# Kernel optimization log

Measured on AMD Instinct MI355X. Metric: run time of the kernel, lower is better.

Reference implementation:

```python
import jax, jax.numpy as jnp
import numpy as np

IN_F = 3072
OUT_F = 3072
SCALE = 1.0
KRON_SIZES = (16, 16, 12)  # q1*q2*q3 == IN_F


def setup_inputs() -> dict:
    key = jax.random.key(0)
    ks = jax.random.split(key, 8)
    x = jax.random.normal(ks[0], (4, 4096, IN_F), dtype=jnp.float32)
    # SVD factors of the frozen linear weight (k = min(out, in) = 3072)
    U = jax.random.normal(ks[1], (OUT_F, OUT_F), dtype=jnp.float32) * 0.02
    S = jax.random.uniform(ks[2], (OUT_F,), dtype=jnp.float32)  # nonnegative singular values
    V = jax.random.normal(ks[3], (OUT_F, IN_F), dtype=jnp.float32) * 0.02
    delta = jnp.full((OUT_F,), 0.001, dtype=jnp.float32)
    q1, q2, q3 = KRON_SIZES
    # initialized as identity in the module; add tiny noise so grads are nontrivial
    Q1 = jnp.eye(q1, dtype=jnp.float32) + 0.01 * jax.random.normal(ks[4], (q1, q1), dtype=jnp.float32)
    Q2 = jnp.eye(q2, dtype=jnp.float32) + 0.01 * jax.random.normal(ks[5], (q2, q2), dtype=jnp.float32)
    Q3 = jnp.eye(q3, dtype=jnp.float32) + 0.01 * jax.random.normal(ks[6], (q3, q3), dtype=jnp.float32)
    return {"x": x, "U": U, "S": S, "V": V, "delta": delta, "Q1": Q1, "Q2": Q2, "Q3": Q3}


def reference(x, U, S, V, delta, Q1, Q2, Q3):
    # S' = relu(S + delta); W = U @ diag(S') @ V  (diag fused as column scaling)
    Sp = jax.nn.relu(S + delta)
    W = (U * Sp[None, :]) @ V                      # [out, in]
    ortho = jnp.kron(jnp.kron(Q1, Q2), Q3)         # [in, in]
    W_t = ortho @ W.T                              # [in, out]
    # F.linear(input, W_t.t()) == input @ W_t ; dropout_p = 0 (inference)
    out = jnp.einsum('bsd,do->bso', x, W_t)
    return out * SCALE
```

## Files before the change

### kernel.cpp

```cpp
#include <hip/hip_runtime.h>

typedef unsigned short u16;
typedef unsigned int u32;
typedef __attribute__((ext_vector_type(8))) __bf16 bf16x8;
typedef __attribute__((ext_vector_type(4))) float f32x4;
typedef __attribute__((ext_vector_type(8))) u16 u16x8;


__device__ __forceinline__ u16 f2bf(float f) {
    union { float f; u32 u; } v; v.f = f;
    u32 r = v.u + 0x7FFFu + ((v.u >> 16) & 1u);
    return (u16)(r >> 16);
}

__device__ __forceinline__ void gload16(const void* g, void* l) {
    __builtin_amdgcn_global_load_lds(
        (const __attribute__((address_space(1))) u32*)g,
        (__attribute__((address_space(3))) u32*)l,
        16, 0, 0);
}

__global__ __launch_bounds__(256) void conv_bf16(
    const float* __restrict__ in, u16* __restrict__ out) {
    const size_t i = (size_t)blockIdx.x * 256 + threadIdx.x;
    const float4 a = ((const float4*)in)[i * 2];
    const float4 b = ((const float4*)in)[i * 2 + 1];
    u16x8 o;
    o[0] = f2bf(a.x); o[1] = f2bf(a.y); o[2] = f2bf(a.z); o[3] = f2bf(a.w);
    o[4] = f2bf(b.x); o[5] = f2bf(b.y); o[6] = f2bf(b.z); o[7] = f2bf(b.w);
    ((u16x8*)out)[i] = o;
}

__global__ __launch_bounds__(64) void conv_scale(
    const float* __restrict__ U, const float* __restrict__ S,
    const float* __restrict__ D, u16* __restrict__ out) {
    const int m = blockIdx.y;
    const int k = (blockIdx.x * 64 + threadIdx.x) * 8;
    const size_t base = (size_t)m * 3072 + k;
    const float4 a = *(const float4*)&U[base];
    const float4 b = *(const float4*)&U[base + 4];
    const float4 s1 = *(const float4*)&S[k], s2 = *(const float4*)&S[k + 4];
    const float4 d1 = *(const float4*)&D[k], d2 = *(const float4*)&D[k + 4];
    u16x8 o;
    o[0] = f2bf(a.x * fmaxf(s1.x + d1.x, 0.f));
    o[1] = f2bf(a.y * fmaxf(s1.y + d1.y, 0.f));
    o[2] = f2bf(a.z * fmaxf(s1.z + d1.z, 0.f));
    o[3] = f2bf(a.w * fmaxf(s1.w + d1.w, 0.f));
    o[4] = f2bf(b.x * fmaxf(s2.x + d2.x, 0.f));
    o[5] = f2bf(b.y * fmaxf(s2.y + d2.y, 0.f));
    o[6] = f2bf(b.z * fmaxf(s2.z + d2.z, 0.f));
    o[7] = f2bf(b.w * fmaxf(s2.w + d2.w, 0.f));
    *(u16x8*)&out[base] = o;
}

__global__ __launch_bounds__(256) void transpose_conv(
    const float* __restrict__ V, u16* __restrict__ Vt, int n) {
    __shared__ float tile[64][65];
    const int k0 = blockIdx.y * 64, j0 = blockIdx.x * 64;
    const int t = threadIdx.x;
    const int r = t >> 4, c4 = t & 15;
#pragma unroll
    for (int i = 0; i < 4; i++) {
        int row = i * 16 + r;
        const float4 v = *(const float4*)&V[(size_t)(k0 + row) * n + j0 + c4 * 4];
        tile[row][c4 * 4 + 0] = v.x;
        tile[row][c4 * 4 + 1] = v.y;
        tile[row][c4 * 4 + 2] = v.z;
        tile[row][c4 * 4 + 3] = v.w;
    }
    __syncthreads();
#pragma unroll
    for (int i = 0; i < 4; i++) {
        int row = i * 16 + r;
        ushort4 o;
        o.x = f2bf(tile[c4 * 4 + 0][row]);
        o.y = f2bf(tile[c4 * 4 + 1][row]);
        o.z = f2bf(tile[c4 * 4 + 2][row]);
        o.w = f2bf(tile[c4 * 4 + 3][row]);
        *(ushort4*)&Vt[(size_t)(j0 + row) * n + k0 + c4 * 4] = o;
    }
}

__global__ __launch_bounds__(512, 2) void gemm256(
    const u16* __restrict__ A, const u16* __restrict__ B,
    float* __restrict__ C, int M, int N, int K) {
    __shared__ u16 As[2][16384];
    __shared__ u16 Bs[2][16384];
    const int t = threadIdx.x;

    const int nbx = gridDim.x;
    const int bid = blockIdx.y * nbx + blockIdx.x;
    const int cpx = (nbx * gridDim.y) >> 3;
    const int sid = (bid & 7) * cpx + (bid >> 3);
    const int m0 = (sid / nbx) * 256, n0 = (sid % nbx) * 256;

    const int lane = t & 63, quad = lane >> 4, lrow = lane & 15;
    const int wave = t >> 6, wr = wave >> 2, wc = wave & 3;

    const int schunk = (t & 7) ^ ((t >> 3) & 7);
    const u16* Ag = A + (size_t)(m0 + (t >> 3)) * K + schunk * 8;
    const u16* Bg = B + (size_t)(n0 + (t >> 3)) * K + schunk * 8;

    const int sl = quad ^ (lrow & 7);
    const int aoff = (wr * 128 + lrow) * 64 + sl * 8;
    const int boff = (wc * 64 + lrow) * 64 + sl * 8;

    f32x4 acc[8][4] = {};

#define STGA(dst, q, kbe) gload16(Ag + (size_t)(q) * 64 * K + (kbe), (char*)(dst) + (q) * 8192 + t * 16)
#define STGB(dst, q, kbe) gload16(Bg + (size_t)(q) * 64 * K + (kbe), (char*)(dst) + (q) * 8192 + t * 16)

    const int NT = K >> 6;
    STGA(As[0], 0, 0); STGA(As[0], 1, 0); STGA(As[0], 2, 0); STGA(As[0], 3, 0);
    STGB(Bs[0], 0, 0); STGB(Bs[0], 1, 0); STGB(Bs[0], 2, 0); STGB(Bs[0], 3, 0);
    if (NT > 1) {
        STGA(As[1], 0, 64); STGA(As[1], 2, 64);
        STGB(Bs[1], 0, 64); STGB(Bs[1], 1, 64);
        asm volatile("s_waitcnt vmcnt(4)" ::: "memory");
    } else {
        asm volatile("s_waitcnt vmcnt(0)" ::: "memory");
    }
    __builtin_amdgcn_s_barrier();

    for (int tt = 0; tt < NT; ++tt) {
        const int b = tt & 1;
        const u16* Acur = As[b];
        const u16* Bcur = Bs[b];
        u16* Anxt = As[b ^ 1];
        u16* Bnxt = Bs[b ^ 1];
        bf16x8 bq[4], aq[4];

#define PHASE_TAIL(OFF)                                                       \
        __builtin_amdgcn_s_barrier();                                         \
        asm volatile("s_waitcnt lgkmcnt(0)" ::: "memory");                    \
        __builtin_amdgcn_sched_barrier(0);                                    \
        __builtin_amdgcn_s_setprio(1);                                        \
        _Pragma("unroll")                                                     \
        for (int mi = 0; mi < 4; mi++)                                        \
            _Pragma("unroll")                                                 \
            for (int ni = 0; ni < 4; ni++)                                    \
                acc[mi + OFF][ni] = __builtin_amdgcn_mfma_f32_16x16x32_bf16(  \
                    aq[mi], bq[ni], acc[mi + OFF][ni], 0, 0, 0);              \
        __builtin_amdgcn_s_setprio(0);

#pragma unroll
        for (int ni = 0; ni < 4; ni++) bq[ni] = *(const bf16x8*)&Bcur[boff + ni * 1024];
#pragma unroll
        for (int mi = 0; mi < 4; mi++) aq[mi] = *(const bf16x8*)&Acur[aoff + mi * 1024];
        if (tt + 1 < NT) { STGA(Anxt, 1, (tt + 1) * 64); STGA(Anxt, 3, (tt + 1) * 64); }
        PHASE_TAIL(0)
        __builtin_amdgcn_s_barrier();

#pragma unroll
        for (int mi = 0; mi < 4; mi++) aq[mi] = *(const bf16x8*)&Acur[aoff + (mi + 4) * 1024];
        if (tt + 1 < NT) { STGB(Bnxt, 2, (tt + 1) * 64); STGB(Bnxt, 3, (tt + 1) * 64); }
        PHASE_TAIL(4)
        __builtin_amdgcn_s_barrier();

#pragma unroll
        for (int ni = 0; ni < 4; ni++) bq[ni] = *(const bf16x8*)&Bcur[(boff + ni * 1024) ^ 32];
#pragma unroll
        for (int mi = 0; mi < 4; mi++) aq[mi] = *(const bf16x8*)&Acur[(aoff + mi * 1024) ^ 32];
        PHASE_TAIL(0)
        __builtin_amdgcn_s_barrier();

#pragma unroll
        for (int mi = 0; mi < 4; mi++) aq[mi] = *(const bf16x8*)&Acur[(aoff + (mi + 4) * 1024) ^ 32];
        if (tt + 2 < NT) {
            STGA((u16*)Acur, 0, (tt + 2) * 64); STGA((u16*)Acur, 2, (tt + 2) * 64);
            STGB((u16*)Bcur, 0, (tt + 2) * 64); STGB((u16*)Bcur, 1, (tt + 2) * 64);
        }
        PHASE_TAIL(4)
        if (tt + 2 < NT)
            asm volatile("s_waitcnt vmcnt(4)" ::: "memory");
        else
            asm volatile("s_waitcnt vmcnt(0)" ::: "memory");
        __builtin_amdgcn_s_barrier();
#undef PHASE_TAIL
    }
#undef STGA
#undef STGB

#pragma unroll
    for (int mi = 0; mi < 8; mi++) {
#pragma unroll
        for (int rr = 0; rr < 4; rr++) {
            const int row = m0 + wr * 128 + mi * 16 + quad * 4 + rr;
            float* cp = C + (size_t)row * N + n0 + wc * 64 + lrow;
#pragma unroll
            for (int ni = 0; ni < 4; ni++) cp[ni * 16] = acc[mi][ni][rr];
        }
    }
}

__global__ __launch_bounds__(256) void kron_apply(
    const float* __restrict__ W, const float* __restrict__ Q1,
    const float* __restrict__ Q2, const float* __restrict__ Q3,
    u16* __restrict__ WtT) {
    __shared__ float T0[3072], T1[3072];
    __shared__ float Q1s[256], Q2s[256], Q3s[144];
    const int o = blockIdx.x, t = threadIdx.x;
#pragma unroll
    for (int i = 0; i < 12; i++) T0[t + i * 256] = W[(size_t)o * 3072 + t + i * 256];
    Q1s[t] = Q1[t];
    Q2s[t] = Q2[t];
    if (t < 144) Q3s[t] = Q3[t];
    __syncthreads();
#pragma unroll
    for (int i = 0; i < 12; i++) {
        int e = t + i * 256;
        int d1 = e / 192, rem = e % 192;
        float s = 0.f;
#pragma unroll
        for (int j1 = 0; j1 < 16; j1++) s += Q1s[d1 * 16 + j1] * T0[j1 * 192 + rem];
        T1[e] = s;
    }
    __syncthreads();
#pragma unroll
    for (int i = 0; i < 12; i++) {
        int e = t + i * 256;
        int j3 = e % 12, d2 = (e / 12) & 15, d1 = e / 192;
        float s = 0.f;
#pragma unroll
        for (int j2 = 0; j2 < 16; j2++) s += Q2s[d2 * 16 + j2] * T1[d1 * 192 + j2 * 12 + j3];
        T0[e] = s;
    }
    __syncthreads();
#pragma unroll
    for (int i = 0; i < 12; i++) {
        int e = t + i * 256;
        int d3 = e % 12, b = e - d3;
        float s = 0.f;
#pragma unroll
        for (int j3 = 0; j3 < 12; j3++) s += Q3s[d3 * 12 + j3] * T0[b + j3];
        WtT[(size_t)o * 3072 + e] = f2bf(s);
    }
}

extern "C" void kernel_launch(void* const* d_in, const int* in_sizes, int n_in,
                              void* d_out, int out_size, void* d_ws, size_t ws_size,
                              hipStream_t stream) {
    const float* x   = (const float*)d_in[0];
    const float* U   = (const float*)d_in[1];
    const float* S   = (const float*)d_in[2];
    const float* V   = (const float*)d_in[3];
    const float* dl  = (const float*)d_in[4];
    const float* Q1  = (const float*)d_in[5];
    const float* Q2  = (const float*)d_in[6];
    const float* Q3  = (const float*)d_in[7];
    float* out = (float*)d_out;

    char* ws = (char*)d_ws;
    u16*   xb  = (u16*)ws;
    u16*   Ub  = (u16*)(ws + 100663296);
    u16*   Vt  = (u16*)(ws + 100663296 + 18874368);
    float* W   = (float*)(ws + 100663296 + 2 * 18874368);
    u16*   WtT = Ub;

    hipLaunchKernelGGL(conv_bf16, dim3(24576), dim3(256), 0, stream, x, xb);
    hipLaunchKernelGGL(conv_scale, dim3(6, 3072), dim3(64), 0, stream, U, S, dl, Ub);
    hipLaunchKernelGGL(transpose_conv, dim3(48, 48), dim3(256), 0, stream, V, Vt, 3072);
    hipLaunchKernelGGL(gemm256, dim3(12, 12), dim3(512), 0, stream,
                       Ub, Vt, W, 3072, 3072, 3072);
    hipLaunchKernelGGL(kron_apply, dim3(3072), dim3(256), 0, stream, W, Q1, Q2, Q3, WtT);
    hipLaunchKernelGGL(gemm256, dim3(12, 64), dim3(512), 0, stream,
                       xb, WtT, out, 16384, 3072, 3072);
}
```

Before: 850.1 us.

## Fuse fp32-to-bf16 conversion of x into main GEMM A-tile loads

Drops the separate conversion kernel that wrote a bf16 copy of x. The main GEMM now loads fp32 x tiles into registers, converts them, and writes them to LDS while the current tile's MFMAs run. B tiles keep the async global-to-LDS path. The weight-building GEMM is also moved to a simpler 128x128 single-buffered kernel with a larger grid. The fused path reads twice the bytes of A per tile and adds register pressure, VALU conversion work and explicit LDS writes inside the pipelined loop.

```diff
diff --git a/kernel.cpp b/kernel.cpp
--- a/kernel.cpp
+++ b/kernel.cpp
@@ -20,15 +20,11 @@
         16, 0, 0);
 }
 
-__global__ __launch_bounds__(256) void conv_bf16(
-    const float* __restrict__ in, u16* __restrict__ out) {
-    const size_t i = (size_t)blockIdx.x * 256 + threadIdx.x;
-    const float4 a = ((const float4*)in)[i * 2];
-    const float4 b = ((const float4*)in)[i * 2 + 1];
+__device__ __forceinline__ void cvt_wr(u16* dst, float4 a, float4 b) {
     u16x8 o;
     o[0] = f2bf(a.x); o[1] = f2bf(a.y); o[2] = f2bf(a.z); o[3] = f2bf(a.w);
     o[4] = f2bf(b.x); o[5] = f2bf(b.y); o[6] = f2bf(b.z); o[7] = f2bf(b.w);
-    ((u16x8*)out)[i] = o;
+    *(u16x8*)dst = o;
 }
 
 __global__ __launch_bounds__(64) void conv_scale(
@@ -81,8 +77,64 @@
     }
 }
 
-__global__ __launch_bounds__(512, 2) void gemm256(
+__global__ __launch_bounds__(256) void gemm_bt(
     const u16* __restrict__ A, const u16* __restrict__ B,
+    float* __restrict__ C, int M, int N, int K) {
+    __shared__ u16 As[128 * 64];
+    __shared__ u16 Bs[128 * 64];
+    const int t = threadIdx.x;
+    const int m0 = blockIdx.y * 128, n0 = blockIdx.x * 128;
+    const int wave = t >> 6, lane = t & 63;
+    const int quad = lane >> 4, lrow = lane & 15;
+    const int wm = (wave >> 1) * 64, wn = (wave & 1) * 64;
+    const int gr = t >> 3;
+    const int gc = (t & 7) ^ (gr & 7);
+    const int c0 = (quad ^ (lrow & 7)) * 8;
+    f32x4 acc[4][4] = {};
+
+    const u16* Ag = A + (size_t)(m0 + gr) * K + gc * 8;
+    const u16* Bg = B + (size_t)(n0 + gr) * K + gc * 8;
+
+    for (int kb = 0; kb < K; kb += 64) {
+#pragma unroll
+        for (int i = 0; i < 4; i++) {
+            gload16(Ag + (size_t)i * 32 * K + kb, (char*)As + i * 4096 + t * 16);
+            gload16(Bg + (size_t)i * 32 * K + kb, (char*)Bs + i * 4096 + t * 16);
+        }
+        __syncthreads();
+#pragma unroll
+        for (int kk = 0; kk < 2; kk++) {
+            const int co = c0 ^ (kk * 32);
+            bf16x8 af[4], bfr[4];
+#pragma unroll
+            for (int mi = 0; mi < 4; mi++)
+                af[mi] = *(const bf16x8*)&As[(wm + mi * 16 + lrow) * 64 + co];
+#pragma unroll
+            for (int ni = 0; ni < 4; ni++)
+                bfr[ni] = *(const bf16x8*)&Bs[(wn + ni * 16 + lrow) * 64 + co];
+#pragma unroll
+            for (int mi = 0; mi < 4; mi++)
+#pragma unroll
+                for (int ni = 0; ni < 4; ni++)
+                    acc[mi][ni] = __builtin_amdgcn_mfma_f32_16x16x32_bf16(
+                        af[mi], bfr[ni], acc[mi][ni], 0, 0, 0);
+        }
+        __syncthreads();
+    }
+#pragma unroll
+    for (int mi = 0; mi < 4; mi++) {
+#pragma unroll
+        for (int rr = 0; rr < 4; rr++) {
+            int row = m0 + wm + mi * 16 + quad * 4 + rr;
+            float* cp = C + (size_t)row * N + n0 + wn + lrow;
+#pragma unroll
+            for (int ni = 0; ni < 4; ni++) cp[ni * 16] = acc[mi][ni][rr];
+        }
+    }
+}
+
+__global__ __launch_bounds__(512, 2) void gemm256_xa(
+    const float* __restrict__ A, const u16* __restrict__ B,
     float* __restrict__ C, int M, int N, int K) {
     __shared__ u16 As[2][16384];
     __shared__ u16 Bs[2][16384];
@@ -98,8 +150,8 @@
     const int wave = t >> 6, wr = wave >> 2, wc = wave & 3;
 
     const int schunk = (t & 7) ^ ((t >> 3) & 7);
-    const u16* Ag = A + (size_t)(m0 + (t >> 3)) * K + schunk * 8;
-    const u16* Bg = B + (size_t)(n0 + (t >> 3)) * K + schunk * 8;
+    const float* Axf = A + (size_t)(m0 + (t >> 3)) * K + schunk * 8;
+    const u16*   Bg  = B + (size_t)(n0 + (t >> 3)) * K + schunk * 8;
 
     const int sl = quad ^ (lrow & 7);
     const int aoff = (wr * 128 + lrow) * 64 + sl * 8;
@@ -107,28 +159,32 @@
 
     f32x4 acc[8][4] = {};
 
-#define STGA(dst, q, kbe) gload16(Ag + (size_t)(q) * 64 * K + (kbe), (char*)(dst) + (q) * 8192 + t * 16)
 #define STGB(dst, q, kbe) gload16(Bg + (size_t)(q) * 64 * K + (kbe), (char*)(dst) + (q) * 8192 + t * 16)
 
     const int NT = K >> 6;
-    STGA(As[0], 0, 0); STGA(As[0], 1, 0); STGA(As[0], 2, 0); STGA(As[0], 3, 0);
     STGB(Bs[0], 0, 0); STGB(Bs[0], 1, 0); STGB(Bs[0], 2, 0); STGB(Bs[0], 3, 0);
-    if (NT > 1) {
-        STGA(As[1], 0, 64); STGA(As[1], 2, 64);
-        STGB(Bs[1], 0, 64); STGB(Bs[1], 1, 64);
-        asm volatile("s_waitcnt vmcnt(4)" ::: "memory");
-    } else {
-        asm volatile("s_waitcnt vmcnt(0)" ::: "memory");
-    }
+    if (NT > 1) { STGB(Bs[1], 0, 64); STGB(Bs[1], 1, 64); }
+#pragma unroll
+    for (int q = 0; q < 4; q++) {
+        const float* p = Axf + (size_t)q * 64 * K;
+        float4 x0 = *(const float4*)p;
+        float4 x1 = *(const float4*)(p + 4);
+        cvt_wr(&As[0][q * 4096 + t * 8], x0, x1);
+    }
+    if (NT > 1) asm volatile("s_waitcnt vmcnt(2)" ::: "memory");
+    else        asm volatile("s_waitcnt vmcnt(0)" ::: "memory");
+    asm volatile("s_waitcnt lgkmcnt(0)" ::: "memory");
     __builtin_amdgcn_s_barrier();
 
     for (int tt = 0; tt < NT; ++tt) {
         const int b = tt & 1;
         const u16* Acur = As[b];
         const u16* Bcur = Bs[b];
-        u16* Anxt = As[b ^ 1];
-        u16* Bnxt = Bs[b ^ 1];
+        u16* Anx = As[b ^ 1];
+        u16* Bnx = Bs[b ^ 1];
         bf16x8 bq[4], aq[4];
+        float4 a0, a1, a2, a3;
+        float4 c0, c1, c2, c3;
 
 #define PHASE_TAIL(OFF)                                                       \
         __builtin_amdgcn_s_barrier();                                         \
@@ -147,13 +203,23 @@
         for (int ni = 0; ni < 4; ni++) bq[ni] = *(const bf16x8*)&Bcur[boff + ni * 1024];
 #pragma unroll
         for (int mi = 0; mi < 4; mi++) aq[mi] = *(const bf16x8*)&Acur[aoff + mi * 1024];
-        if (tt + 1 < NT) { STGA(Anxt, 1, (tt + 1) * 64); STGA(Anxt, 3, (tt + 1) * 64); }
+        if (tt + 1 < NT) {
+            const float* p = Axf + (size_t)(tt + 1) * 64;
+            a0 = *(const float4*)p;
+            a1 = *(const float4*)(p + 4);
+            a2 = *(const float4*)(p + (size_t)64 * K);
+            a3 = *(const float4*)(p + (size_t)64 * K + 4);
+        }
         PHASE_TAIL(0)
         __builtin_amdgcn_s_barrier();
 
 #pragma unroll
         for (int mi = 0; mi < 4; mi++) aq[mi] = *(const bf16x8*)&Acur[aoff + (mi + 4) * 1024];
-        if (tt + 1 < NT) { STGB(Bnxt, 2, (tt + 1) * 64); STGB(Bnxt, 3, (tt + 1) * 64); }
+        if (tt + 1 < NT) {
+            STGB(Bnx, 2, (tt + 1) * 64); STGB(Bnx, 3, (tt + 1) * 64);
+            cvt_wr(&Anx[0 * 4096 + t * 8], a0, a1);
+            cvt_wr(&Anx[1 * 4096 + t * 8], a2, a3);
+        }
         PHASE_TAIL(4)
         __builtin_amdgcn_s_barrier();
 
@@ -161,24 +227,31 @@
         for (int ni = 0; ni < 4; ni++) bq[ni] = *(const bf16x8*)&Bcur[(boff + ni * 1024) ^ 32];
 #pragma unroll
         for (int mi = 0; mi < 4; mi++) aq[mi] = *(const bf16x8*)&Acur[(aoff + mi * 1024) ^ 32];
+        if (tt + 1 < NT) {
+            const float* p = Axf + (size_t)(tt + 1) * 64 + (size_t)128 * K;
+            c0 = *(const float4*)p;
+            c1 = *(const float4*)(p + 4);
+            c2 = *(const float4*)(p + (size_t)64 * K);
+            c3 = *(const float4*)(p + (size_t)64 * K + 4);
+        }
         PHASE_TAIL(0)
         __builtin_amdgcn_s_barrier();
 
 #pragma unroll
         for (int mi = 0; mi < 4; mi++) aq[mi] = *(const bf16x8*)&Acur[(aoff + (mi + 4) * 1024) ^ 32];
-        if (tt + 2 < NT) {
-            STGA((u16*)Acur, 0, (tt + 2) * 64); STGA((u16*)Acur, 2, (tt + 2) * 64);
-            STGB((u16*)Bcur, 0, (tt + 2) * 64); STGB((u16*)Bcur, 1, (tt + 2) * 64);
+        if (tt + 2 < NT) { STGB((u16*)Bcur, 0, (tt + 2) * 64); STGB((u16*)Bcur, 1, (tt + 2) * 64); }
+        if (tt + 1 < NT) {
+            cvt_wr(&Anx[2 * 4096 + t * 8], c0, c1);
+            cvt_wr(&Anx[3 * 4096 + t * 8], c2, c3);
         }
         PHASE_TAIL(4)
         if (tt + 2 < NT)
-            asm volatile("s_waitcnt vmcnt(4)" ::: "memory");
+            asm volatile("s_waitcnt vmcnt(2)" ::: "memory");
         else
             asm volatile("s_waitcnt vmcnt(0)" ::: "memory");
         __builtin_amdgcn_s_barrier();
 #undef PHASE_TAIL
     }
-#undef STGA
 #undef STGB
 
 #pragma unroll
@@ -251,18 +324,16 @@
     float* out = (float*)d_out;
 
     char* ws = (char*)d_ws;
-    u16*   xb  = (u16*)ws;
-    u16*   Ub  = (u16*)(ws + 100663296);
-    u16*   Vt  = (u16*)(ws + 100663296 + 18874368);
-    float* W   = (float*)(ws + 100663296 + 2 * 18874368);
+    u16*   Ub  = (u16*)ws;
+    u16*   Vt  = (u16*)(ws + 18874368);
+    float* W   = (float*)(ws + 2 * 18874368);
     u16*   WtT = Ub;
 
-    hipLaunchKernelGGL(conv_bf16, dim3(24576), dim3(256), 0, stream, x, xb);
     hipLaunchKernelGGL(conv_scale, dim3(6, 3072), dim3(64), 0, stream, U, S, dl, Ub);
     hipLaunchKernelGGL(transpose_conv, dim3(48, 48), dim3(256), 0, stream, V, Vt, 3072);
-    hipLaunchKernelGGL(gemm256, dim3(12, 12), dim3(512), 0, stream,
+    hipLaunchKernelGGL(gemm_bt, dim3(24, 24), dim3(256), 0, stream,
                        Ub, Vt, W, 3072, 3072, 3072);
     hipLaunchKernelGGL(kron_apply, dim3(3072), dim3(256), 0, stream, W, Q1, Q2, Q3, WtT);
-    hipLaunchKernelGGL(gemm256, dim3(12, 64), dim3(512), 0, stream,
-                       xb, WtT, out, 16384, 3072, 3072);
-}
+    hipLaunchKernelGGL(gemm256_xa, dim3(12, 64), dim3(512), 0, stream,
+                       x, WtT, out, 16384, 3072, 3072);
+}
```

Measured after the change: 989.4 us. +16.4%, slower.
